# Performance work log

Measured on AMD Instinct MI355X. Metric: run time of the kernel, lower is better.

Reference implementation:

```python
import jax, jax.numpy as jnp
import numpy as np

B, T, I, H, K, C, TH, CLS = 128, 512, 300, 150, 6, 300, 20, 5

def setup_inputs() -> dict:
    key = jax.random.key(0)
    ks = jax.random.split(key, 16)
    s = lambda *sh: 1.0 / np.sqrt(sh[-1])
    inp = {
        "x": jax.random.normal(ks[0], (B, T, I), jnp.float32),
        # GRU params (PyTorch layout: [3H, in]) for fwd/bwd directions
        "Wih_f": jax.random.normal(ks[1], (3 * H, I), jnp.float32) * s(3 * H, I),
        "Whh_f": jax.random.normal(ks[2], (3 * H, H), jnp.float32) * s(3 * H, H),
        "bih_f": jax.random.normal(ks[3], (3 * H,), jnp.float32) * 0.01,
        "bhh_f": jax.random.normal(ks[4], (3 * H,), jnp.float32) * 0.01,
        "Wih_b": jax.random.normal(ks[5], (3 * H, I), jnp.float32) * s(3 * H, I),
        "Whh_b": jax.random.normal(ks[6], (3 * H, H), jnp.float32) * s(3 * H, H),
        "bih_b": jax.random.normal(ks[7], (3 * H,), jnp.float32) * 0.01,
        "bhh_b": jax.random.normal(ks[8], (3 * H,), jnp.float32) * 0.01,
        # topic attention params (stacked over K topics)
        "attn_context": jax.random.normal(ks[9], (K, C), jnp.float32),
        "Wattn": jax.random.normal(ks[10], (K, C + 2 * H, 2 * H), jnp.float32) * s(1, C + 2 * H),
        "battn": jax.random.normal(ks[11], (K, 2 * H), jnp.float32) * 0.01,
        "Wtop": jax.random.normal(ks[12], (K, 2 * H, TH), jnp.float32) * s(1, 2 * H),
        "btop": jax.random.normal(ks[13], (K, TH), jnp.float32) * 0.01,
        "Wout": jax.random.normal(ks[14], (K * TH, CLS), jnp.float32) * s(1, K * TH),
        "bout": jax.random.normal(ks[15], (CLS,), jnp.float32) * 0.01,
    }
    return inp

def _gru_dir(x, Wih, Whh, bih, bhh, reverse):
    # x: [B,T,I] -> outputs [B,T,H], final hidden [B,H]
    xT = jnp.swapaxes(x, 0, 1)                    # [T,B,I]
    if reverse:
        xT = xT[::-1]
    gi = xT @ Wih.T + bih                         # [T,B,3H] input projections (one big GEMM)
    h0 = jnp.zeros((x.shape[0], Whh.shape[1]), x.dtype)
    def step(h, g):
        gh = h @ Whh.T + bhh
        i_r, i_z, i_n = jnp.split(g, 3, axis=-1)
        h_r, h_z, h_n = jnp.split(gh, 3, axis=-1)
        r = jax.nn.sigmoid(i_r + h_r)
        z = jax.nn.sigmoid(i_z + h_z)
        n = jnp.tanh(i_n + r * h_n)
        h_new = (1.0 - z) * n + z * h
        return h_new, h_new
    hT, ys = jax.lax.scan(step, h0, gi)
    if reverse:
        ys = ys[::-1]
    return jnp.swapaxes(ys, 0, 1), hT

def reference(x, Wih_f, Whh_f, bih_f, bhh_f, Wih_b, Whh_b, bih_b, bhh_b,
              attn_context, Wattn, battn, Wtop, btop, Wout, bout):
    # eval mode: dropout is identity
    out_f, h_f = _gru_dir(x, Wih_f, Whh_f, bih_f, bhh_f, False)
    out_b, h_b = _gru_dir(x, Wih_b, Whh_b, bih_b, bhh_b, True)
    seq = jnp.concatenate([out_f, out_b], axis=-1)       # [B,T,2H]
    hidden = jnp.concatenate([h_f, h_b], axis=-1)        # [B,2H]
    Bsz = x.shape[0]
    Kt = attn_context.shape[0]
    # per-topic context: cat(context_k, hidden) -> linear -> tanh, batched over topics
    ctx_in = jnp.concatenate([
        jnp.broadcast_to(attn_context[None, :, :], (Bsz, Kt, attn_context.shape[1])),
        jnp.broadcast_to(hidden[:, None, :], (Bsz, Kt, hidden.shape[1])),
    ], axis=-1)                                          # [B,K,C+2H]
    context = jnp.tanh(jnp.einsum('bkc,kcd->bkd', ctx_in, Wattn) + battn)  # [B,K,2H]
    # attention pooling over time, all topics at once
    energy = jnp.einsum('btd,bkd->btk', seq, context)    # [B,T,K]
    probs = jax.nn.softmax(energy, axis=1)
    pooled = jnp.einsum('btd,btk->bkd', seq, probs)      # [B,K,2H]
    topic = jax.nn.relu(jnp.einsum('bkd,kdh->bkh', pooled, Wtop) + btop)   # [B,K,TH]
    feats = topic.reshape(Bsz, -1)                       # [B,K*TH]
    logits = feats @ Wout + bout
    out = jax.nn.softmax(logits, axis=1)                 # eval + validate=False path
    # regularization loss on normalized contexts
    nc = context / jnp.linalg.norm(context, axis=2, keepdims=True).clip(1e-12)
    G = jnp.einsum('bkd,bjd->bkj', nc, nc)               # [B,K,K]
    diff = G - jnp.eye(Kt, dtype=G.dtype)[None]
    reg = jnp.mean(jnp.sqrt(jnp.sum(diff * diff, axis=(1, 2))))
    return out, reg
```

## Files before the change

### kernel.cpp

```cpp
#include <hip/hip_runtime.h>
#include <hip/hip_bf16.h>
#include <math.h>

#define Bq   128
#define Tq   512
#define Iq   300
#define Hq   150
#define G3   450
#define Kq   6
#define Cq   300
#define D2   300
#define THq  20
#define CLSq 5

typedef __attribute__((ext_vector_type(8))) short short8;
typedef __attribute__((ext_vector_type(4))) float floatx4;

__global__ __launch_bounds__(256) void cast_bf16_kernel(
    const float* __restrict__ in, __hip_bfloat16* __restrict__ out, int n4)
{
    const int i = blockIdx.x * 256 + threadIdx.x;
    if (i < n4) {
        float4 v = *(const float4*)(in + 4 * (size_t)i);
        out[4 * (size_t)i + 0] = __float2bfloat16(v.x);
        out[4 * (size_t)i + 1] = __float2bfloat16(v.y);
        out[4 * (size_t)i + 2] = __float2bfloat16(v.z);
        out[4 * (size_t)i + 3] = __float2bfloat16(v.w);
    }
}

#define LB 40

__global__ __launch_bounds__(256) void gi_gemm_mfma(
    const __hip_bfloat16* __restrict__ xb,
    const __hip_bfloat16* __restrict__ Wbf,
    const float* __restrict__ bf_, const float* __restrict__ bb_,
    float* __restrict__ gic, int t0f, int t0b, int tcShift)
{
    const int dir = blockIdx.z;
    const unsigned short* W = (const unsigned short*)(Wbf + (size_t)dir * G3 * Iq);
    const unsigned short* X = (const unsigned short*)xb;
    const float* bias = dir ? bb_ : bf_;
    const int t0 = dir ? t0b : t0f;
    const int TCr = 1 << tcShift;
    float* outb = gic + (size_t)dir * Bq * TCr * G3;

    const int m0 = blockIdx.y * 128;
    const int n0 = blockIdx.x * 128;
    const int tid  = threadIdx.x;
    const int wv   = tid >> 6, lane = tid & 63;
    const int wm   = wv & 1,  wn   = wv >> 1;
    const int quad = lane >> 4, mr = lane & 15;

    __shared__ __align__(16) unsigned short Ab[128 * LB];
    __shared__ __align__(16) unsigned short Bb[128 * LB];

    floatx4 acc[4][4];
    #pragma unroll
    for (int i = 0; i < 4; ++i)
        #pragma unroll
        for (int j = 0; j < 4; ++j)
            acc[i][j] = (floatx4){0.f, 0.f, 0.f, 0.f};

    for (int k0 = 0; k0 < 320; k0 += 32) {
        __syncthreads();
        #pragma unroll
        for (int i = 0; i < 4; ++i) {
            const int g = tid + 256 * i;
            const int row = g >> 3, kq = g & 7;
            const int k = k0 + kq * 4;
            const int r = m0 + row;
            const int bb2 = r >> tcShift, lt = r & (TCr - 1);
            ushort4 av = make_ushort4(0, 0, 0, 0);
            if (k < Iq)
                av = *(const ushort4*)(X + ((size_t)bb2 * Tq + t0 + lt) * Iq + k);
            *(ushort4*)&Ab[row * LB + kq * 4] = av;
            const int n = n0 + row;
            ushort4 bv = make_ushort4(0, 0, 0, 0);
            if (n < G3 && k < Iq)
                bv = *(const ushort4*)(W + (size_t)n * Iq + k);
            *(ushort4*)&Bb[row * LB + kq * 4] = bv;
        }
        __syncthreads();

        short8 af[4], bfr[4];
        #pragma unroll
        for (int i = 0; i < 4; ++i)
            af[i] = *(const short8*)&Ab[(wm * 64 + i * 16 + mr) * LB + quad * 8];
        #pragma unroll
        for (int j = 0; j < 4; ++j)
            bfr[j] = *(const short8*)&Bb[(wn * 64 + j * 16 + mr) * LB + quad * 8];
        #pragma unroll
        for (int i = 0; i < 4; ++i)
            #pragma unroll
            for (int j = 0; j < 4; ++j)
                acc[i][j] = __builtin_amdgcn_mfma_f32_16x16x32_bf16(
                    af[i], bfr[j], acc[i][j], 0, 0, 0);
    }

    #pragma unroll
    for (int j = 0; j < 4; ++j) {
        const int gn = n0 + wn * 64 + j * 16 + mr;
        if (gn >= G3) continue;
        const float bv = bias[gn];
        #pragma unroll
        for (int i = 0; i < 4; ++i) {
            const int mbase = m0 + wm * 64 + i * 16 + quad * 4;
            #pragma unroll
            for (int rg = 0; rg < 4; ++rg)
                outb[(size_t)(mbase + rg) * G3 + gn] = acc[i][j][rg] + bv;
        }
    }
}

template<int CTRL>
__device__ __forceinline__ float qadd(float v) {
    return v + __int_as_float(__builtin_amdgcn_update_dpp(
        0, __float_as_int(v), CTRL, 0xF, 0xF, true));
}

__global__ __launch_bounds__(640) void gru_rec(
    const float* __restrict__ gic,
    const float* __restrict__ Whh_f, const float* __restrict__ bhh_f,
    const float* __restrict__ Whh_b, const float* __restrict__ bhh_b,
    float* __restrict__ hstate,
    float* __restrict__ seq,
    int chunk, int tcShift)
{
    const int TCr = 1 << tcShift;
    const int bid = blockIdx.x;
    const int dir = bid & 1;
    const int b   = bid >> 1;
    const float* Whh = dir ? Whh_b : Whh_f;
    const float* bhh = dir ? bhh_b : bhh_f;
    const int tid = threadIdx.x;
    const int t   = tid >> 2;
    const int p   = tid & 3;
    const bool act = (t < Hq);

    __shared__ __align__(16) float stage[64 * 150];
    __shared__ __align__(16) float hbufs[2][160];

    float w0[40], w1[40], w2[40];
    const int c0 = p * 38;
    const int cmax = (p == 3) ? 36 : 38;
    if (act) {
        #pragma unroll
        for (int c = 0; c < 40; ++c) {
            const bool v = (c < cmax);
            const int col = c0 + (v ? c : 0);
            w0[c] = v ? Whh[(size_t)t * Hq + col] : 0.f;
            w1[c] = v ? Whh[(size_t)(Hq + t) * Hq + col] : 0.f;
            w2[c] = v ? Whh[(size_t)(2 * Hq + t) * Hq + col] : 0.f;
        }
    }

    float bhv = 0.f;
    if (act && p < 3) bhv = bhh[p * Hq + t];
    const int gidx = (p == 0) ? t : (p == 1) ? (Hq + t) : (2 * Hq + t);
    const bool gload = act && (p != 2);

    float* hs = hstate + (size_t)(dir * Bq + b) * Hq;
    float hprev = 0.f;
    if (act && chunk > 0) hprev = hs[t];

    if (tid < 320) {
        const int buf = tid / 160, o = tid - buf * 160;
        const int pp = o / 40, off = o % 40;
        const int j = pp * 38 + off;
        hbufs[buf][o] = (off < 38 && j < Hq && chunk > 0) ? hs[j] : 0.f;
    }
    __syncthreads();

    const float* gib = gic + (size_t)(dir * Bq + b) * TCr * G3;
    const int t0 = dir ? (Tq - TCr * (chunk + 1)) : (chunk * TCr);
    float* seqb = seq + (size_t)b * Tq * D2 + dir * Hq;
    const int hslot = (t / 38) * 40 + (t % 38);

    const int lt0 = dir ? (TCr - 1) : 0;
    float gval = gload ? gib[(size_t)lt0 * G3 + gidx] : 0.f;

    int cur = 0;
    for (int s = 0; s < TCr; ++s) {
        const int ltn = dir ? (TCr - 2 - s) : (s + 1);
        float gnext = 0.f;
        if (s + 1 < TCr && gload)
            gnext = gib[(size_t)ltn * G3 + gidx];

        if (act) {
            const float base = bhv + gval;
            float a0 = (p == 0) ? base : 0.f;
            float a1 = (p == 1) ? base : 0.f;
            float a2 = (p == 2) ? base : 0.f;
            float a3 = (p == 3) ? base : 0.f;
            const float4* hq = (const float4*)&hbufs[cur][p * 40];
            #pragma unroll
            for (int q = 0; q < 10; ++q) {
                const float4 hv = hq[q];
                a0 += hv.x * w0[4*q]   + hv.y * w0[4*q+1]
                    + hv.z * w0[4*q+2] + hv.w * w0[4*q+3];
                a1 += hv.x * w1[4*q]   + hv.y * w1[4*q+1]
                    + hv.z * w1[4*q+2] + hv.w * w1[4*q+3];
                a2 += hv.x * w2[4*q]   + hv.y * w2[4*q+1]
                    + hv.z * w2[4*q+2] + hv.w * w2[4*q+3];
            }
            a0 = qadd<0xB1>(a0); a1 = qadd<0xB1>(a1);
            a2 = qadd<0xB1>(a2); a3 = qadd<0xB1>(a3);
            a0 = qadd<0x4E>(a0); a1 = qadd<0x4E>(a1);
            a2 = qadd<0x4E>(a2); a3 = qadd<0x4E>(a3);

            const float r  = 1.f / (1.f + __expf(-a0));
            const float z  = 1.f / (1.f + __expf(-a1));
            const float nv = tanhf(a3 + r * a2);
            const float hn = (1.f - z) * nv + z * hprev;
            hprev = hn;
            if (p == 0) {
                hbufs[cur ^ 1][hslot] = hn;
                stage[(s & 63) * 150 + t] = hn;
            }
        }
        __syncthreads();

        if ((s & 63) == 63 || s == TCr - 1) {
            const int sf0 = s & ~63;
            const int nf2 = (s - sf0 + 1) * 75;
            for (int idx = tid; idx < nf2; idx += 640) {
                const int rrow = idx / 75, cc = idx % 75;
                const int ss = sf0 + rrow;
                const int ltw = dir ? (TCr - 1 - ss) : ss;
                *(float2*)(seqb + (size_t)(t0 + ltw) * D2 + 2 * cc) =
                    *(const float2*)&stage[rrow * 150 + 2 * cc];
            }
            __syncthreads();
        }

        gval = gnext;
        cur ^= 1;
    }

    if (act && p == 0) hs[t] = hprev;
}

__global__ void ctxw_kernel(
    const float* __restrict__ attn_context,
    const float* __restrict__ Wattn,
    const float* __restrict__ battn,
    float* __restrict__ ctxW)
{
    const int o = blockIdx.x * 256 + threadIdx.x;
    if (o >= Kq * D2) return;
    const int k = o / D2, d = o % D2;
    float acc = battn[o];
    const float* Wp = Wattn + ((size_t)k * (Cq + D2)) * D2 + d;
    for (int c = 0; c < Cq; ++c)
        acc += attn_context[k * Cq + c] * Wp[(size_t)c * D2];
    ctxW[o] = acc;
}

__global__ __launch_bounds__(256) void ctx_compute(
    const float* __restrict__ seq,
    const float* __restrict__ Wattn,
    const float* __restrict__ ctxW,
    float* __restrict__ context,
    float* __restrict__ normsq)
{
    const int b = blockIdx.x;
    const int k = blockIdx.y;
    const int tid = threadIdx.x;
    const int lane = tid & 63, wv = tid >> 6;

    __shared__ float hb[304];
    __shared__ float red[4];

    for (int i = tid; i < D2; i += 256)
        hb[i] = (i < Hq) ? seq[((size_t)b * Tq + (Tq - 1)) * D2 + i]
                         : seq[(size_t)b * Tq * D2 + i];
    __syncthreads();

    float ssq = 0.f;
    for (int d = tid; d < D2; d += 256) {
        float acc = ctxW[k * D2 + d];
        const float* Wp = Wattn + ((size_t)k * (Cq + D2) + Cq) * D2 + d;
        for (int jj = 0; jj < D2; ++jj)
            acc += hb[jj] * Wp[(size_t)jj * D2];
        const float c = tanhf(acc);
        context[((size_t)b * Kq + k) * D2 + d] = c;
        ssq += c * c;
    }
    for (int off = 32; off > 0; off >>= 1) ssq += __shfl_xor(ssq, off, 64);
    if (lane == 0) red[wv] = ssq;
    __syncthreads();
    if (tid == 0) normsq[b * Kq + k] = red[0] + red[1] + red[2] + red[3];
}

__global__ __launch_bounds__(256) void gram_kernel(
    const float* __restrict__ context,
    const float* __restrict__ normsq,
    float* __restrict__ regbuf)
{
    const int b = blockIdx.x;
    const int tid = threadIdx.x;
    __shared__ float ctx[Kq * D2];
    __shared__ float Gm[36];

    for (int o = tid; o < Kq * D2; o += 256)
        ctx[o] = context[(size_t)b * Kq * D2 + o];
    __syncthreads();

    if (tid < 36) {
        const int k = tid / 6, jj = tid % 6;
        float g = 0.f;
        for (int d = 0; d < D2; ++d)
            g += ctx[k * D2 + d] * ctx[jj * D2 + d];
        const float nk = fmaxf(sqrtf(normsq[b * Kq + k]), 1e-12f);
        const float nj = fmaxf(sqrtf(normsq[b * Kq + jj]), 1e-12f);
        g /= (nk * nj);
        const float diff = g - ((k == jj) ? 1.f : 0.f);
        Gm[tid] = diff * diff;
    }
    __syncthreads();
    if (tid == 0) {
        float s = 0.f;
        for (int i = 0; i < 36; ++i) s += Gm[i];
        regbuf[b] = sqrtf(s);
    }
}

__global__ __launch_bounds__(256) void energy_kernel(
    const float* __restrict__ seq,
    const float* __restrict__ context,
    float* __restrict__ en)
{
    const int tc = blockIdx.x;
    const int b  = blockIdx.y;
    const int tid = threadIdx.x;
    const int lane = tid & 63, wv = tid >> 6;

    __shared__ float ctx[Kq * D2];
    for (int o = tid; o < Kq * D2; o += 256)
        ctx[o] = context[(size_t)b * Kq * D2 + o];
    __syncthreads();

    const float* seqb = seq + (size_t)b * Tq * D2;
    for (int s = 0; s < 16; ++s) {
        const int tt = tc * 64 + s * 4 + wv;
        float acc[Kq] = {0.f,0.f,0.f,0.f,0.f,0.f};
        for (int d = lane; d < D2; d += 64) {
            const float sv = seqb[(size_t)tt * D2 + d];
            #pragma unroll
            for (int k = 0; k < Kq; ++k) acc[k] += sv * ctx[k * D2 + d];
        }
        #pragma unroll
        for (int k = 0; k < Kq; ++k) {
            float v = acc[k];
            for (int off = 32; off > 0; off >>= 1) v += __shfl_xor(v, off, 64);
            if (lane == 0) en[((size_t)b * Tq + tt) * Kq + k] = v;
        }
    }
}

__global__ __launch_bounds__(256) void softmax_kernel(float* __restrict__ en)
{
    const int b = blockIdx.x;
    const int tid = threadIdx.x;
    const int lane = tid & 63, wv = tid >> 6;
    __shared__ float es[Tq * Kq];
    __shared__ float red[8];

    for (int o = tid; o < Tq * Kq; o += 256)
        es[o] = en[(size_t)b * Tq * Kq + o];
    __syncthreads();

    for (int k = 0; k < Kq; ++k) {
        float m = -1e30f;
        for (int tt = tid; tt < Tq; tt += 256) m = fmaxf(m, es[tt * Kq + k]);
        for (int off = 32; off > 0; off >>= 1) m = fmaxf(m, __shfl_xor(m, off, 64));
        if (lane == 0) red[wv] = m;
        __syncthreads();
        m = fmaxf(fmaxf(red[0], red[1]), fmaxf(red[2], red[3]));
        float ssum = 0.f;
        for (int tt = tid; tt < Tq; tt += 256) {
            const float e = __expf(es[tt * Kq + k] - m);
            es[tt * Kq + k] = e;
            ssum += e;
        }
        for (int off = 32; off > 0; off >>= 1) ssum += __shfl_xor(ssum, off, 64);
        if (lane == 0) red[4 + wv] = ssum;
        __syncthreads();
        const float inv = 1.f / (red[4] + red[5] + red[6] + red[7]);
        for (int tt = tid; tt < Tq; tt += 256) es[tt * Kq + k] *= inv;
        __syncthreads();
    }

    for (int o = tid; o < Tq * Kq; o += 256)
        en[(size_t)b * Tq * Kq + o] = es[o];
}

__global__ __launch_bounds__(256) void pooledp_kernel(
    const float* __restrict__ seq,
    const float* __restrict__ en,
    float* __restrict__ partial)
{
    const int tc = blockIdx.x;
    const int b  = blockIdx.y;
    const int tid = threadIdx.x;
    const int lane = tid & 63, wv = tid >> 6;

    __shared__ float pr[64 * Kq];
    __shared__ float part[4][Kq * D2];

    if (tid < 64 * Kq / 2) {
        pr[tid]       = en[((size_t)b * Tq + tc * 64) * Kq + tid];
        pr[tid + 192] = en[((size_t)b * Tq + tc * 64) * Kq + tid + 192];
    }
    __syncthreads();

    const float* seqb = seq + (size_t)b * Tq * D2;

    float pp[Kq][5];
    #pragma unroll
    for (int k = 0; k < Kq; ++k)
        #pragma unroll
        for (int q = 0; q < 5; ++q) pp[k][q] = 0.f;

    for (int s = 0; s < 16; ++s) {
        const int tl = s * 4 + wv;
        const int tt = tc * 64 + tl;
        float prr[Kq];
        #pragma unroll
        for (int k = 0; k < Kq; ++k) prr[k] = pr[tl * Kq + k];
        #pragma unroll
        for (int q = 0; q < 5; ++q) {
            const int d = lane + q * 64;
            const float sv = (d < D2) ? seqb[(size_t)tt * D2 + d] : 0.f;
            #pragma unroll
            for (int k = 0; k < Kq; ++k) pp[k][q] += prr[k] * sv;
        }
    }
    #pragma unroll
    for (int k = 0; k < Kq; ++k)
        #pragma unroll
        for (int q = 0; q < 5; ++q) {
            const int d = lane + q * 64;
            if (d < D2) part[wv][k * D2 + d] = pp[k][q];
        }
    __syncthreads();
    float* op = partial + ((size_t)b * 8 + tc) * (Kq * D2);
    for (int o = tid; o < Kq * D2; o += 256)
        op[o] = part[0][o] + part[1][o] + part[2][o] + part[3][o];
}

__global__ __launch_bounds__(256) void final_kernel(
    const float* __restrict__ partial,
    const float* __restrict__ Wtop,
    const float* __restrict__ btop,
    const float* __restrict__ Wout,
    const float* __restrict__ bout,
    float* __restrict__ outp)
{
    const int b = blockIdx.x;
    const int tid = threadIdx.x;
    __shared__ float pooled[Kq * D2];
    __shared__ float feats[Kq * THq];
    __shared__ float lsm[8];

    for (int o = tid; o < Kq * D2; o += 256) {
        float s = 0.f;
        #pragma unroll
        for (int c = 0; c < 8; ++c)
            s += partial[((size_t)b * 8 + c) * (Kq * D2) + o];
        pooled[o] = s;
    }
    __syncthreads();

    if (tid < Kq * THq) {
        const int k = tid / THq, hh = tid % THq;
        float acc = btop[tid];
        const float* wp = Wtop + (size_t)k * D2 * THq + hh;
        for (int d = 0; d < D2; ++d)
            acc += pooled[k * D2 + d] * wp[(size_t)d * THq];
        feats[tid] = fmaxf(acc, 0.f);
    }
    __syncthreads();

    if (tid < CLSq) {
        float acc = bout[tid];
        for (int f = 0; f < Kq * THq; ++f)
            acc += feats[f] * Wout[f * CLSq + tid];
        lsm[tid] = acc;
    }
    __syncthreads();
    if (tid < CLSq) {
        float m = lsm[0];
        for (int c = 1; c < CLSq; ++c) m = fmaxf(m, lsm[c]);
        float s = 0.f;
        for (int c = 0; c < CLSq; ++c) s += __expf(lsm[c] - m);
        outp[(size_t)b * CLSq + tid] = __expf(lsm[tid] - m) / s;
    }
}

__global__ void reg_final(const float* __restrict__ regbuf, float* __restrict__ outp)
{
    const int tid = threadIdx.x;
    float v = regbuf[tid];
    for (int off = 32; off > 0; off >>= 1) v += __shfl_xor(v, off, 64);
    __shared__ float r2[2];
    if ((tid & 63) == 0) r2[tid >> 6] = v;
    __syncthreads();
    if (tid == 0) outp[Bq * CLSq] = (r2[0] + r2[1]) * (1.f / (float)Bq);
}

extern "C" void kernel_launch(void* const* d_in, const int* in_sizes, int n_in,
                              void* d_out, int out_size, void* d_ws, size_t ws_size,
                              hipStream_t stream)
{
    const float* x     = (const float*)d_in[0];
    const float* Wih_f = (const float*)d_in[1];
    const float* Whh_f = (const float*)d_in[2];
    const float* bih_f = (const float*)d_in[3];
    const float* bhh_f = (const float*)d_in[4];
    const float* Wih_b = (const float*)d_in[5];
    const float* Whh_b = (const float*)d_in[6];
    const float* bih_b = (const float*)d_in[7];
    const float* bhh_b = (const float*)d_in[8];
    const float* attn_context = (const float*)d_in[9];
    const float* Wattn = (const float*)d_in[10];
    const float* battn = (const float*)d_in[11];
    const float* Wtop  = (const float*)d_in[12];
    const float* btop  = (const float*)d_in[13];
    const float* Wout  = (const float*)d_in[14];
    const float* bout  = (const float*)d_in[15];
    float* outp = (float*)d_out;

    float* ws       = (float*)d_ws;
    float* seqv     = ws;
    float* hstate   = seqv + (size_t)Bq * Tq * D2;
    float* ctxW     = hstate + (size_t)2 * Bq * Hq;
    float* context  = ctxW + Kq * D2;
    float* regbuf   = context + (size_t)Bq * Kq * D2;
    float* normsq   = regbuf + Bq;
    float* en       = normsq + Bq * Kq;
    float* partial  = en + (size_t)Bq * Tq * Kq;
    __hip_bfloat16* xb16 = (__hip_bfloat16*)(partial + (size_t)Bq * 8 * Kq * D2);
    __hip_bfloat16* Wb16 = xb16 + (size_t)Bq * Tq * Iq;
    float* gi_chunk = (float*)(Wb16 + (size_t)2 * G3 * Iq);
    const size_t fixed_floats = (size_t)(gi_chunk - ws);

    int tcShift = 5;
    for (int sh = 8; sh >= 5; --sh) {
        size_t need = (fixed_floats + (size_t)115200 * (1 << sh)) * 4;
        if (need <= ws_size) { tcShift = sh; break; }
    }
    const int TCr = 1 << tcShift;
    const int NL = Tq / TCr;

    cast_bf16_kernel<<<dim3((Bq * Tq * Iq / 4 + 255) / 256), 256, 0, stream>>>(
        x, xb16, Bq * Tq * Iq / 4);
    cast_bf16_kernel<<<dim3((G3 * Iq / 4 + 255) / 256), 256, 0, stream>>>(
        Wih_f, Wb16, G3 * Iq / 4);
    cast_bf16_kernel<<<dim3((G3 * Iq / 4 + 255) / 256), 256, 0, stream>>>(
        Wih_b, Wb16 + (size_t)G3 * Iq, G3 * Iq / 4);

    for (int c = 0; c < NL; ++c) {
        const int t0f = c * TCr;
        const int t0b = Tq - TCr * (c + 1);
        gi_gemm_mfma<<<dim3(4, Bq * TCr / 128, 2), 256, 0, stream>>>(
            xb16, Wb16, bih_f, bih_b, gi_chunk, t0f, t0b, tcShift);
        gru_rec<<<dim3(2 * Bq), 640, 0, stream>>>(
            gi_chunk, Whh_f, bhh_f, Whh_b, bhh_b, hstate, seqv, c, tcShift);
    }

    ctxw_kernel<<<dim3((Kq * D2 + 255) / 256), 256, 0, stream>>>(
        attn_context, Wattn, battn, ctxW);
    ctx_compute<<<dim3(Bq, Kq), 256, 0, stream>>>(seqv, Wattn, ctxW, context, normsq);
    gram_kernel<<<dim3(Bq), 256, 0, stream>>>(context, normsq, regbuf);
    energy_kernel<<<dim3(8, Bq), 256, 0, stream>>>(seqv, context, en);
    softmax_kernel<<<dim3(Bq), 256, 0, stream>>>(en);
    pooledp_kernel<<<dim3(8, Bq), 256, 0, stream>>>(seqv, en, partial);
    final_kernel<<<dim3(Bq), 256, 0, stream>>>(partial, Wtop, btop, Wout, bout, outp);
    reg_final<<<dim3(1), 128, 0, stream>>>(regbuf, outp);
}
```

Measured before the change: 1.296 ms.

## Restructure GRU recurrence to one thread per gate row with shared-memory gate exchange

The recurrent GRU kernel now assigns one thread to each of the 450 gate rows of Whh. Each thread holds its full 150-wide weight row in registers and computes a complete dot product, replacing the old scheme of four threads per hidden unit with DPP quad reductions. The r/z pre-activations pass through shared memory to 150 gate threads, and the block shrinks from 640 to 512 threads with a two-blocks-per-CU launch bound. The aim is to drop the cross-lane reduction and the double-buffered hidden state, but each step now has a longer serial FMA chain and an extra barrier. The ~150-float weight array per thread under that launch bound also risks register spills.

```diff
diff --git a/kernel.cpp b/kernel.cpp
--- a/kernel.cpp
+++ b/kernel.cpp
@@ -113,13 +113,7 @@
     }
 }
 
-template<int CTRL>
-__device__ __forceinline__ float qadd(float v) {
-    return v + __int_as_float(__builtin_amdgcn_update_dpp(
-        0, __float_as_int(v), CTRL, 0xF, 0xF, true));
-}
-
-__global__ __launch_bounds__(640) void gru_rec(
+__global__ __launch_bounds__(512, 2) void gru_rec(
     const float* __restrict__ gic,
     const float* __restrict__ Whh_f, const float* __restrict__ bhh_f,
     const float* __restrict__ Whh_b, const float* __restrict__ bhh_b,
@@ -134,111 +128,93 @@
     const float* Whh = dir ? Whh_b : Whh_f;
     const float* bhh = dir ? bhh_b : bhh_f;
     const int tid = threadIdx.x;
-    const int t   = tid >> 2;
-    const int p   = tid & 3;
-    const bool act = (t < Hq);
+    const bool gemv = (tid < G3);
+    const bool gate = (tid >= 300 && tid < G3);
+    const int t = tid - 300;
 
     __shared__ __align__(16) float stage[64 * 150];
-    __shared__ __align__(16) float hbufs[2][160];
-
-    float w0[40], w1[40], w2[40];
-    const int c0 = p * 38;
-    const int cmax = (p == 3) ? 36 : 38;
-    if (act) {
-        #pragma unroll
-        for (int c = 0; c < 40; ++c) {
-            const bool v = (c < cmax);
-            const int col = c0 + (v ? c : 0);
-            w0[c] = v ? Whh[(size_t)t * Hq + col] : 0.f;
-            w1[c] = v ? Whh[(size_t)(Hq + t) * Hq + col] : 0.f;
-            w2[c] = v ? Whh[(size_t)(2 * Hq + t) * Hq + col] : 0.f;
-        }
-    }
-
-    float bhv = 0.f;
-    if (act && p < 3) bhv = bhh[p * Hq + t];
-    const int gidx = (p == 0) ? t : (p == 1) ? (Hq + t) : (2 * Hq + t);
-    const bool gload = act && (p != 2);
+    __shared__ __align__(16) float hbuf[152];
+    __shared__ float sArr[300];
+
+    float w[152];
+    w[150] = 0.f; w[151] = 0.f;
+    if (gemv) {
+        const float* wr = Whh + (size_t)tid * Hq;
+        #pragma unroll
+        for (int q = 0; q < 75; ++q) {
+            const float2 v = *(const float2*)(wr + 2 * q);
+            w[2 * q]     = v.x;
+            w[2 * q + 1] = v.y;
+        }
+    } else {
+        #pragma unroll
+        for (int c = 0; c < 150; ++c) w[c] = 0.f;
+    }
+    const float bh = gemv ? bhh[tid] : 0.f;
 
     float* hs = hstate + (size_t)(dir * Bq + b) * Hq;
     float hprev = 0.f;
-    if (act && chunk > 0) hprev = hs[t];
-
-    if (tid < 320) {
-        const int buf = tid / 160, o = tid - buf * 160;
-        const int pp = o / 40, off = o % 40;
-        const int j = pp * 38 + off;
-        hbufs[buf][o] = (off < 38 && j < Hq && chunk > 0) ? hs[j] : 0.f;
-    }
+    if (gate && chunk > 0) hprev = hs[t];
+
+    if (tid < 152)
+        hbuf[tid] = (tid < Hq && chunk > 0) ? hs[tid] : 0.f;
     __syncthreads();
 
     const float* gib = gic + (size_t)(dir * Bq + b) * TCr * G3;
     const int t0 = dir ? (Tq - TCr * (chunk + 1)) : (chunk * TCr);
     float* seqb = seq + (size_t)b * Tq * D2 + dir * Hq;
-    const int hslot = (t / 38) * 40 + (t % 38);
+    const float4* hb4 = (const float4*)hbuf;
 
     const int lt0 = dir ? (TCr - 1) : 0;
-    float gval = gload ? gib[(size_t)lt0 * G3 + gidx] : 0.f;
-
-    int cur = 0;
+    float gval = gemv ? gib[(size_t)lt0 * G3 + tid] : 0.f;
+
     for (int s = 0; s < TCr; ++s) {
         const int ltn = dir ? (TCr - 2 - s) : (s + 1);
         float gnext = 0.f;
-        if (s + 1 < TCr && gload)
-            gnext = gib[(size_t)ltn * G3 + gidx];
-
-        if (act) {
-            const float base = bhv + gval;
-            float a0 = (p == 0) ? base : 0.f;
-            float a1 = (p == 1) ? base : 0.f;
-            float a2 = (p == 2) ? base : 0.f;
-            float a3 = (p == 3) ? base : 0.f;
-            const float4* hq = (const float4*)&hbufs[cur][p * 40];
+        if (s + 1 < TCr && gemv)
+            gnext = gib[(size_t)ltn * G3 + tid];
+
+        float ghn = 0.f;
+        if (gemv) {
+            float acc = bh + ((tid < 300) ? gval : 0.f);
             #pragma unroll
-            for (int q = 0; q < 10; ++q) {
-                const float4 hv = hq[q];
-                a0 += hv.x * w0[4*q]   + hv.y * w0[4*q+1]
-                    + hv.z * w0[4*q+2] + hv.w * w0[4*q+3];
-                a1 += hv.x * w1[4*q]   + hv.y * w1[4*q+1]
-                    + hv.z * w1[4*q+2] + hv.w * w1[4*q+3];
-                a2 += hv.x * w2[4*q]   + hv.y * w2[4*q+1]
-                    + hv.z * w2[4*q+2] + hv.w * w2[4*q+3];
+            for (int q = 0; q < 38; ++q) {
+                const float4 hv = hb4[q];
+                acc += hv.x * w[4*q]   + hv.y * w[4*q+1]
+                     + hv.z * w[4*q+2] + hv.w * w[4*q+3];
             }
-            a0 = qadd<0xB1>(a0); a1 = qadd<0xB1>(a1);
-            a2 = qadd<0xB1>(a2); a3 = qadd<0xB1>(a3);
-            a0 = qadd<0x4E>(a0); a1 = qadd<0x4E>(a1);
-            a2 = qadd<0x4E>(a2); a3 = qadd<0x4E>(a3);
-
-            const float r  = 1.f / (1.f + __expf(-a0));
-            const float z  = 1.f / (1.f + __expf(-a1));
-            const float nv = tanhf(a3 + r * a2);
+            if (tid < 300) sArr[tid] = acc;
+            else           ghn = acc;
+        }
+        __syncthreads();
+
+        if (gate) {
+            const float r  = 1.f / (1.f + __expf(-sArr[t]));
+            const float z  = 1.f / (1.f + __expf(-sArr[150 + t]));
+            const float nv = tanhf(gval + r * ghn);
             const float hn = (1.f - z) * nv + z * hprev;
             hprev = hn;
-            if (p == 0) {
-                hbufs[cur ^ 1][hslot] = hn;
-                stage[(s & 63) * 150 + t] = hn;
-            }
+            hbuf[t] = hn;
+            stage[(s & 63) * 150 + t] = hn;
         }
         __syncthreads();
 
         if ((s & 63) == 63 || s == TCr - 1) {
             const int sf0 = s & ~63;
             const int nf2 = (s - sf0 + 1) * 75;
-            for (int idx = tid; idx < nf2; idx += 640) {
+            for (int idx = tid; idx < nf2; idx += 512) {
                 const int rrow = idx / 75, cc = idx % 75;
                 const int ss = sf0 + rrow;
                 const int ltw = dir ? (TCr - 1 - ss) : ss;
                 *(float2*)(seqb + (size_t)(t0 + ltw) * D2 + 2 * cc) =
                     *(const float2*)&stage[rrow * 150 + 2 * cc];
             }
-            __syncthreads();
         }
 
         gval = gnext;
-        cur ^= 1;
-    }
-
-    if (act && p == 0) hs[t] = hprev;
+    }
+
+    if (gate) hs[t] = hprev;
 }
 
 __global__ void ctxw_kernel(
@@ -566,7 +542,7 @@
         const int t0b = Tq - TCr * (c + 1);
         gi_gemm_mfma<<<dim3(4, Bq * TCr / 128, 2), 256, 0, stream>>>(
             xb16, Wb16, bih_f, bih_b, gi_chunk, t0f, t0b, tcShift);
-        gru_rec<<<dim3(2 * Bq), 640, 0, stream>>>(
+        gru_rec<<<dim3(2 * Bq), 512, 0, stream>>>(
             gi_chunk, Whh_f, bhh_f, Whh_b, bhh_b, hstate, seqv, c, tcShift);
     }
 
```

New measurement: 1.254 ms. 1.03x faster.
